# Performance work log

Hardware: AMD Instinct MI355X
Metric: run time of the kernel (lower is better)

Reference implementation:

```python
import jax, jax.numpy as jnp
import numpy as np

# Solver constants matching init_kwargs
DX = 2.0 / 128.0        # c_delta_x (domain [-1,1], 128 coarse cells)
DT = 1e-3               # c_delta_t
T_STAR = 0.064          # delta_t_star
NT = int(round(T_STAR / DT))  # 64 velocity-Verlet steps


def peri_laplacian(v, dx):
    """5-point Laplacian with periodic BC on last two axes."""
    return (jnp.roll(v, 1, -1) - 2.0 * v + jnp.roll(v, -1, -1)
            + jnp.roll(v, 1, -2) - 2.0 * v + jnp.roll(v, -1, -2)) / (dx * dx)


def grad2func(vx, vy, dx, sumv):
    """Recover u from its gradient components (wx, wy) via FFT inversion.
    vx, vy: [B, H, W]; sumv sets the DC (mean) mode."""
    ny, nx = vx.shape[-2], vx.shape[-1]
    kx = (2.0 * jnp.pi) * jnp.fft.fftfreq(nx, d=dx).astype(vx.dtype)  # [W]
    ky = (2.0 * jnp.pi) * jnp.fft.fftfreq(ny, d=dx).astype(vx.dtype)  # [H]
    KX = kx[None, :]
    KY = ky[:, None]
    rad = KX ** 2 + KY ** 2
    rad = rad.at[0, 0].set(1.0)
    hatx = jnp.fft.fft2(vx)
    haty = jnp.fft.fft2(vy)
    hatv = -1j * (hatx * KX + haty * KY) / rad
    hatv = hatv.at[..., 0, 0].set(sumv.astype(hatv.dtype))
    return jnp.real(jnp.fft.ifft2(hatv))


def wave_sol_from_energy(wx, wy, wtc, c, dx, sumv):
    u = grad2func(wx, wy, dx, sumv)
    ut = wtc * c
    return u, ut


def velocity_verlet(u, ut, c, dx, dt, nt):
    """nt steps of velocity Verlet for u_tt = c^2 * Lap(u), periodic BC."""
    c2 = c * c
    def step(carry, _):
        u, ut = carry
        lap0 = peri_laplacian(u, dx)
        u_new = u + dt * ut + 0.5 * dt * dt * c2 * lap0
        lap1 = peri_laplacian(u_new, dx)
        ut_new = ut + 0.5 * dt * c2 * (lap0 + lap1)
        return (u_new, ut_new), None
    (u, ut), _ = jax.lax.scan(step, (u, ut), None, length=nt)
    return u, ut


def wave_energy_components(u, ut, c, dx):
    wx = jnp.zeros_like(u).at[..., :, 1:].set((u[..., :, 1:] - u[..., :, :-1]) / dx)
    wy = jnp.zeros_like(u).at[..., 1:, :].set((u[..., 1:, :] - u[..., :-1, :]) / dx)
    wtc = ut / c
    return wx, wy, wtc


def setup_inputs() -> dict:
    key = jax.random.key(0)
    k1, k2 = jax.random.split(key)
    B, H, W = 16, 256, 256
    # channels 0..2: energy components (small-amplitude fields)
    fields = 0.1 * jax.random.normal(k1, (B, 3, H, W), dtype=jnp.float32)
    # channel 3: wave speed, strictly positive (divided by / squared in solver)
    vel = jax.random.uniform(k2, (B, 1, H, W), dtype=jnp.float32,
                             minval=1.0, maxval=3.0)
    restr_output = jnp.concatenate([fields, vel], axis=1)  # [B, 4, H, W]
    return {"restr_output": restr_output}


def reference(restr_output) -> jnp.ndarray:
    wx = restr_output[:, 0]
    wy = restr_output[:, 1]
    wtc = restr_output[:, 2]
    vel_c = restr_output[:, 3]
    # faithful to original: scalar sum of wx over the ENTIRE batch
    sumv = jnp.sum(wx)
    u, ut = wave_sol_from_energy(wx, wy, wtc, vel_c, DX, sumv)
    u, ut = velocity_verlet(u, ut, vel_c, DX, DT, NT)
    wx2, wy2, wtc2 = wave_energy_components(u, ut, vel_c, DX)
    return jnp.stack((wx2, wy2, wtc2, vel_c), axis=1)  # [B, 4, H, W]
```

## Files before the change

kernel.cpp:

```cpp
#include <hip/hip_runtime.h>

#define NBATCH 16
#define NPIX   65536
#define NTOT   (NBATCH * NPIX)

constexpr float DTf    = 0.001f;
constexpr float HDTf   = 0.0005f;
constexpr float HDT2f  = 5.0000000000000004e-07f;
constexpr float INV_DX  = 64.0f;
constexpr float INV_DX2 = 4096.0f;
constexpr float TWO_PI  = 6.28318530717958647692f;

constexpr int FWD = -1;
constexpr int INV =  1;

__device__ __forceinline__ void fft256_stockham(float* ar, float* ai,
                                                float* br, float* bi,
                                                const float* twr, const float* twi,
                                                int lane)
{
  float *xr = ar, *xi = ai, *yr = br, *yi = bi;
#pragma unroll
  for (int s = 0; s < 8; ++s) {
    const int m = 1 << s;
    __syncthreads();
#pragma unroll
    for (int q = 0; q < 2; ++q) {
      const int b  = lane + (q << 6);
      const int jm = b & ~(m - 1);
      const float wr = twr[jm], wi = twi[jm];
      const float c0r = xr[b],       c0i = xi[b];
      const float c1r = xr[b + 128], c1i = xi[b + 128];
      const int i0 = b + jm, i1 = i0 + m;
      yr[i0] = c0r + c1r;
      yi[i0] = c0i + c1i;
      const float dr = c0r - c1r, di = c0i - c1i;
      yr[i1] = wr * dr - wi * di;
      yi[i1] = wr * di + wi * dr;
    }
    float* t;
    t = xr; xr = yr; yr = t;
    t = xi; xi = yi; yi = t;
  }
  __syncthreads();
}

__global__ __launch_bounds__(512) void k_fwd_rows_pack(const float* __restrict__ in,
                                                       float2* __restrict__ A,
                                                       float* __restrict__ sum)
{
  __shared__ float ar[8 * 256], ai[8 * 256], br[8 * 256], bi[8 * 256];
  __shared__ float twr[128], twi[128];
  __shared__ float part[8];
  const int tid = threadIdx.x;
  const int lane = tid & 63;
  const int wv = tid >> 6;
  const int row0 = blockIdx.x << 3;

  float acc = 0.0f;
  for (int i = tid; i < 2048; i += 512) {
    const int r = i >> 8, e = i & 255;
    const int row = row0 + r;
    const int b = row >> 8, y = row & 255;
    const float vx = in[((size_t)(b << 2) << 16) + (y << 8) + e];
    const float vy = in[((size_t)((b << 2) | 1) << 16) + (y << 8) + e];
    ar[(r << 8) + e] = vx; acc += vx;
    ai[(r << 8) + e] = vy;
  }
  for (int t = tid; t < 128; t += 512) {
    float s, c;
    sincosf((float)FWD * (TWO_PI / 256.0f) * (float)t, &s, &c);
    twr[t] = c; twi[t] = s;
  }
#pragma unroll
  for (int o = 32; o > 0; o >>= 1) acc += __shfl_down(acc, o);
  if (lane == 0) part[wv] = acc;
  __syncthreads();
  if (tid == 0) {
    float s = part[0];
#pragma unroll
    for (int w = 1; w < 8; ++w) s += part[w];
    atomicAdd(sum, s);
  }

  fft256_stockham(ar + (wv << 8), ai + (wv << 8), br + (wv << 8), bi + (wv << 8),
                  twr, twi, lane);

  for (int i = tid; i < 2048; i += 512) {
    const int r = i >> 8, e = i & 255;
    A[((size_t)(row0 + r) << 8) + e] = make_float2(ar[(r << 8) + e], ai[(r << 8) + e]);
  }
}

__global__ __launch_bounds__(512) void k_fft_cols_panel_fwd(float2* __restrict__ X)
{
  constexpr int CS = 260;
  __shared__ float ar[8 * CS], ai[8 * CS], br[8 * CS], bi[8 * CS];
  __shared__ float twr[128], twi[128];
  const int tid = threadIdx.x;
  const int lane = tid & 63;
  const int wv = tid >> 6;
  const int b = blockIdx.x >> 5;
  const int x0 = (blockIdx.x & 31) << 3;
  float2* base = X + ((size_t)b << 16) + x0;

  for (int i = tid; i < 2048; i += 512) {
    const int row = i >> 3, c = i & 7;
    const float2 v = base[(row << 8) + c];
    ar[c * CS + row] = v.x;
    ai[c * CS + row] = v.y;
  }
  for (int t = tid; t < 128; t += 512) {
    float s, c;
    sincosf((float)FWD * (TWO_PI / 256.0f) * (float)t, &s, &c);
    twr[t] = c; twi[t] = s;
  }
  fft256_stockham(ar + wv * CS, ai + wv * CS, br + wv * CS, bi + wv * CS,
                  twr, twi, lane);
  for (int i = tid; i < 2048; i += 512) {
    const int row = i >> 3, c = i & 7;
    base[(row << 8) + c] = make_float2(ar[c * CS + row], ai[c * CS + row]);
  }
}

__global__ __launch_bounds__(512) void k_combine_invcol(const float2* __restrict__ A,
                                                        const float* __restrict__ sum,
                                                        float2* __restrict__ Bf)
{
  constexpr int CS = 260;
  __shared__ float ar[8 * CS], ai[8 * CS], br[8 * CS], bi[8 * CS];
  __shared__ float twr[128], twi[128];
  const int tid = threadIdx.x;
  const int lane = tid & 63;
  const int wv = tid >> 6;
  const int b = blockIdx.x >> 5;
  const int x0 = (blockIdx.x & 31) << 3;
  const float2* Ab = A + ((size_t)b << 16);

  for (int i = tid; i < 2048; i += 512) {
    const int ky = i >> 3, c = i & 7;
    const int kx = x0 + c;
    const float2 Zk = Ab[(ky << 8) + kx];
    const int ky2 = (256 - ky) & 255, kx2 = (256 - kx) & 255;
    const float2 Zm = Ab[(ky2 << 8) + kx2];
    const float Xr = 0.5f * (Zk.x + Zm.x), Xi = 0.5f * (Zk.y - Zm.y);
    const float Yr = 0.5f * (Zk.y + Zm.y), Yi = 0.5f * (Zm.x - Zk.x);
    const float fx = 0.25f * (float)(kx < 128 ? kx : kx - 256);
    const float fy = 0.25f * (float)(ky < 128 ? ky : ky - 256);
    const float kxv = TWO_PI * fx, kyv = TWO_PI * fy;
    float re, im;
    if ((ky | kx) == 0) {
      re = sum[0]; im = 0.0f;
    } else {
      const float rad = kxv * kxv + kyv * kyv;
      const float sr = Xr * kxv + Yr * kyv;
      const float si = Xi * kxv + Yi * kyv;
      re = si / rad; im = -sr / rad;
    }
    ar[c * CS + ky] = re;
    ai[c * CS + ky] = im;
  }
  for (int t = tid; t < 128; t += 512) {
    float s, c;
    sincosf((float)INV * (TWO_PI / 256.0f) * (float)t, &s, &c);
    twr[t] = c; twi[t] = s;
  }
  fft256_stockham(ar + wv * CS, ai + wv * CS, br + wv * CS, bi + wv * CS,
                  twr, twi, lane);
  float2* ob = Bf + ((size_t)b << 16) + x0;
  for (int i = tid; i < 2048; i += 512) {
    const int row = i >> 3, c = i & 7;
    ob[(row << 8) + c] = make_float2(ar[c * CS + row], ai[c * CS + row]);
  }
}

__global__ __launch_bounds__(512) void k_inv_rows_extract(const float2* __restrict__ Bf,
                                                          const float* __restrict__ in,
                                                          float* __restrict__ u,
                                                          float* __restrict__ ut)
{
  __shared__ float ar[8 * 256], ai[8 * 256], br[8 * 256], bi[8 * 256];
  __shared__ float twr[128], twi[128];
  const int tid = threadIdx.x;
  const int lane = tid & 63;
  const int wv = tid >> 6;
  const int row0 = blockIdx.x << 3;

  for (int i = tid; i < 2048; i += 512) {
    const int r = i >> 8, e = i & 255;
    const float2 v = Bf[((size_t)(row0 + r) << 8) + e];
    ar[(r << 8) + e] = v.x;
    ai[(r << 8) + e] = v.y;
  }
  for (int t = tid; t < 128; t += 512) {
    float s, c;
    sincosf((float)INV * (TWO_PI / 256.0f) * (float)t, &s, &c);
    twr[t] = c; twi[t] = s;
  }
  fft256_stockham(ar + (wv << 8), ai + (wv << 8), br + (wv << 8), bi + (wv << 8),
                  twr, twi, lane);

  for (int i = tid; i < 2048; i += 512) {
    const int r = i >> 8, e = i & 255;
    const int row = row0 + r;
    const int b = row >> 8, y = row & 255;
    const float wtc = in[((size_t)((b << 2) | 2) << 16) + (y << 8) + e];
    const float vc  = in[((size_t)((b << 2) | 3) << 16) + (y << 8) + e];
    u [((size_t)row << 8) + e] = ar[(r << 8) + e] * (1.0f / 65536.0f);
    ut[((size_t)row << 8) + e] = wtc * vc;
  }
}

template <int FINAL>
__global__ __launch_bounds__(256, 4) void k_verlet8(const float* __restrict__ u_in,
                                                    const float* __restrict__ ut_in,
                                                    const float* __restrict__ in,
                                                    float* __restrict__ u_out,
                                                    float* __restrict__ ut_out,
                                                    float* __restrict__ out)
{
  __shared__ float su[50 * 51];
  __shared__ float tmp[48 * 49];
  const int tid = threadIdx.x;
  const int b = blockIdx.x >> 6, t = blockIdx.x & 63;
  const int ty0 = (t >> 3) << 5, tx0 = (t & 7) << 5;
  const int ty = tid >> 4, tx = tid & 15;
  const int y0 = 1 + 3 * ty, x0 = 1 + 3 * tx;
  const float* ub  = u_in  + ((size_t)b << 16);
  const float* utb = ut_in + ((size_t)b << 16);
  const float* vb  = in + ((size_t)((b << 2) | 3) << 16);

  for (int i = tid; i < 2500; i += 256) {
    const int iy = i / 50, ix = i - iy * 50;
    const int gy = (ty0 + iy - 9) & 255, gx = (tx0 + ix - 9) & 255;
    su[iy * 51 + ix] = ub[(gy << 8) + gx];
  }
  for (int i = tid; i < 2304; i += 256) {
    const int iy = i / 48, ix = i - iy * 48;
    const int gy = (ty0 + iy - 8) & 255, gx = (tx0 + ix - 8) & 255;
    tmp[iy * 49 + ix] = utb[(gy << 8) + gx];
  }
  __syncthreads();

  float uR[3][3], utR[3][3], c2R[3][3], laR[3][3];
#pragma unroll
  for (int r = 0; r < 3; ++r)
#pragma unroll
    for (int c = 0; c < 3; ++c) {
      uR[r][c]  = su[(y0 + r) * 51 + x0 + c];
      utR[r][c] = tmp[(3 * ty + r) * 49 + 3 * tx + c];
    }
  __syncthreads();
  for (int i = tid; i < 2304; i += 256) {
    const int iy = i / 48, ix = i - iy * 48;
    const int gy = (ty0 + iy - 8) & 255, gx = (tx0 + ix - 8) & 255;
    tmp[iy * 49 + ix] = vb[(gy << 8) + gx];
  }
  __syncthreads();
#pragma unroll
  for (int r = 0; r < 3; ++r)
#pragma unroll
    for (int c = 0; c < 3; ++c) {
      const float cv = tmp[(3 * ty + r) * 49 + 3 * tx + c];
      c2R[r][c] = cv * cv;
    }

  float hN[3], hS[3], hW[3], hE[3];
  auto load_halo = [&]() {
#pragma unroll
    for (int c = 0; c < 3; ++c) {
      hN[c] = su[(y0 - 1) * 51 + x0 + c];
      hS[c] = su[(y0 + 3) * 51 + x0 + c];
    }
#pragma unroll
    for (int r = 0; r < 3; ++r) {
      hW[r] = su[(y0 + r) * 51 + x0 - 1];
      hE[r] = su[(y0 + r) * 51 + x0 + 3];
    }
  };
  auto lap_cell = [&](int r, int c) -> float {
    const float v = uR[r][c];
    const float L = (c == 0) ? hW[r] : uR[r][c - 1];
    const float R = (c == 2) ? hE[r] : uR[r][c + 1];
    const float U = (r == 0) ? hN[c] : uR[r - 1][c];
    const float D = (r == 2) ? hS[c] : uR[r + 1][c];
    const float t2 = 2.0f * v;
    return (((((L - t2) + R) + U) - t2) + D) * INV_DX2;
  };

  load_halo();
#pragma unroll
  for (int r = 0; r < 3; ++r)
#pragma unroll
    for (int c = 0; c < 3; ++c) laR[r][c] = lap_cell(r, c);
  __syncthreads();

  for (int j = 0; j < 8; ++j) {
#pragma unroll
    for (int r = 0; r < 3; ++r)
#pragma unroll
      for (int c = 0; c < 3; ++c)
        uR[r][c] = (uR[r][c] + DTf * utR[r][c]) + (HDT2f * c2R[r][c]) * laR[r][c];
    su[(y0    ) * 51 + x0    ] = uR[0][0];
    su[(y0    ) * 51 + x0 + 1] = uR[0][1];
    su[(y0    ) * 51 + x0 + 2] = uR[0][2];
    su[(y0 + 1) * 51 + x0    ] = uR[1][0];
    su[(y0 + 1) * 51 + x0 + 2] = uR[1][2];
    su[(y0 + 2) * 51 + x0    ] = uR[2][0];
    su[(y0 + 2) * 51 + x0 + 1] = uR[2][1];
    su[(y0 + 2) * 51 + x0 + 2] = uR[2][2];
    __syncthreads();
    load_halo();
#pragma unroll
    for (int r = 0; r < 3; ++r)
#pragma unroll
      for (int c = 0; c < 3; ++c) {
        const float ln = lap_cell(r, c);
        utR[r][c] = utR[r][c] + (HDTf * c2R[r][c]) * (laR[r][c] + ln);
        laR[r][c] = ln;
      }
    __syncthreads();
  }

#pragma unroll
  for (int r = 0; r < 3; ++r)
#pragma unroll
    for (int c = 0; c < 3; ++c) su[(y0 + r) * 51 + x0 + c] = uR[r][c];
  __syncthreads();

  if (FINAL) {
    float wxv[4], wyv[4];
#pragma unroll
    for (int k = 0; k < 4; ++k) {
      const int i = tid + (k << 8);
      const int oy = i >> 5, ox = i & 31;
      const float uc = su[(9 + oy) * 51 + 9 + ox];
      wxv[k] = (tx0 + ox == 0) ? 0.0f : (uc - su[(9 + oy) * 51 + 8 + ox]) * INV_DX;
      wyv[k] = (ty0 + oy == 0) ? 0.0f : (uc - su[(8 + oy) * 51 + 9 + ox]) * INV_DX;
    }
    __syncthreads();
#pragma unroll
    for (int r = 0; r < 3; ++r)
#pragma unroll
      for (int c = 0; c < 3; ++c) su[(y0 + r) * 51 + x0 + c] = utR[r][c];
    __syncthreads();
#pragma unroll
    for (int k = 0; k < 4; ++k) {
      const int i = tid + (k << 8);
      const int oy = i >> 5, ox = i & 31;
      const int g = ((ty0 + oy) << 8) + (tx0 + ox);
      const float utv = su[(9 + oy) * 51 + 9 + ox];
      const float cv  = vb[g];
      out[((size_t)(b << 2) << 16) + g]       = wxv[k];
      out[((size_t)((b << 2) | 1) << 16) + g] = wyv[k];
      out[((size_t)((b << 2) | 2) << 16) + g] = utv / cv;
      out[((size_t)((b << 2) | 3) << 16) + g] = cv;
    }
  } else {
    float* uob  = u_out  + ((size_t)b << 16);
    float* utob = ut_out + ((size_t)b << 16);
    for (int i = tid; i < 1024; i += 256) {
      const int oy = i >> 5, ox = i & 31;
      uob[((ty0 + oy) << 8) + tx0 + ox] = su[(9 + oy) * 51 + 9 + ox];
    }
    __syncthreads();
#pragma unroll
    for (int r = 0; r < 3; ++r)
#pragma unroll
      for (int c = 0; c < 3; ++c) su[(y0 + r) * 51 + x0 + c] = utR[r][c];
    __syncthreads();
    for (int i = tid; i < 1024; i += 256) {
      const int oy = i >> 5, ox = i & 31;
      utob[((ty0 + oy) << 8) + tx0 + ox] = su[(9 + oy) * 51 + 9 + ox];
    }
  }
}

extern "C" void kernel_launch(void* const* d_in, const int* in_sizes, int n_in,
                              void* d_out, int out_size, void* d_ws, size_t ws_size,
                              hipStream_t stream)
{
  const float* in = (const float*)d_in[0];
  float* out = (float*)d_out;
  char* ws = (char*)d_ws;

  float2* A   = (float2*)d_out;
  float*  u1  = (float*)d_out;
  float*  ut1 = u1 + NTOT;
  float2* Bf  = (float2*)((float*)d_out + 2 * NTOT);

  float*  sum = (float*)ws;
  float*  u0  = (float*)ws;
  float*  ut0 = u0 + NTOT;

  hipMemsetAsync(sum, 0, sizeof(float), stream);

  k_fwd_rows_pack<<<NBATCH * 32, 512, 0, stream>>>(in, A, sum);
  k_fft_cols_panel_fwd<<<NBATCH * 32, 512, 0, stream>>>(A);
  k_combine_invcol<<<NBATCH * 32, 512, 0, stream>>>(A, sum, Bf);
  k_inv_rows_extract<<<NBATCH * 32, 512, 0, stream>>>(Bf, in, u1, ut1);

  for (int s = 0; s < 7; ++s) {
    if (s & 1) k_verlet8<0><<<NBATCH * 64, 256, 0, stream>>>(u0, ut0, in, u1, ut1, out);
    else       k_verlet8<0><<<NBATCH * 64, 256, 0, stream>>>(u1, ut1, in, u0, ut0, out);
  }
  k_verlet8<1><<<NBATCH * 64, 256, 0, stream>>>(u0, ut0, in, u1, ut1, out);
}
```

Measured before the change: 259.6 us.

## Fuse column FFT with spectral combine; double-buffer Verlet shared tile

```diff
diff --git a/kernel.cpp b/kernel.cpp
--- a/kernel.cpp
+++ b/kernel.cpp
@@ -92,44 +92,13 @@
   }
 }
 
-__global__ __launch_bounds__(512) void k_fft_cols_panel_fwd(float2* __restrict__ X)
+__global__ __launch_bounds__(1024) void k_cols_fused(const float2* __restrict__ A,
+                                                     const float* __restrict__ sum,
+                                                     float2* __restrict__ Bf)
 {
   constexpr int CS = 260;
-  __shared__ float ar[8 * CS], ai[8 * CS], br[8 * CS], bi[8 * CS];
-  __shared__ float twr[128], twi[128];
-  const int tid = threadIdx.x;
-  const int lane = tid & 63;
-  const int wv = tid >> 6;
-  const int b = blockIdx.x >> 5;
-  const int x0 = (blockIdx.x & 31) << 3;
-  float2* base = X + ((size_t)b << 16) + x0;
-
-  for (int i = tid; i < 2048; i += 512) {
-    const int row = i >> 3, c = i & 7;
-    const float2 v = base[(row << 8) + c];
-    ar[c * CS + row] = v.x;
-    ai[c * CS + row] = v.y;
-  }
-  for (int t = tid; t < 128; t += 512) {
-    float s, c;
-    sincosf((float)FWD * (TWO_PI / 256.0f) * (float)t, &s, &c);
-    twr[t] = c; twi[t] = s;
-  }
-  fft256_stockham(ar + wv * CS, ai + wv * CS, br + wv * CS, bi + wv * CS,
-                  twr, twi, lane);
-  for (int i = tid; i < 2048; i += 512) {
-    const int row = i >> 3, c = i & 7;
-    base[(row << 8) + c] = make_float2(ar[c * CS + row], ai[c * CS + row]);
-  }
-}
-
-__global__ __launch_bounds__(512) void k_combine_invcol(const float2* __restrict__ A,
-                                                        const float* __restrict__ sum,
-                                                        float2* __restrict__ Bf)
-{
-  constexpr int CS = 260;
-  __shared__ float ar[8 * CS], ai[8 * CS], br[8 * CS], bi[8 * CS];
-  __shared__ float twr[128], twi[128];
+  __shared__ float ar[16 * CS], ai[16 * CS], br[16 * CS], bi[16 * CS];
+  __shared__ float twfr[128], twfi[128], twvr[128], twvi[128];
   const int tid = threadIdx.x;
   const int lane = tid & 63;
   const int wv = tid >> 6;
@@ -137,14 +106,31 @@
   const int x0 = (blockIdx.x & 31) << 3;
   const float2* Ab = A + ((size_t)b << 16);
 
-  for (int i = tid; i < 2048; i += 512) {
+  for (int i = tid; i < 4096; i += 1024) {
+    const int row = i >> 4, c = i & 15;
+    const int col = (c < 8) ? (x0 + c) : ((256 - (x0 + (c - 8))) & 255);
+    const float2 v = Ab[(row << 8) + col];
+    ar[c * CS + row] = v.x;
+    ai[c * CS + row] = v.y;
+  }
+  for (int t = tid; t < 128; t += 1024) {
+    float s, c;
+    sincosf((float)FWD * (TWO_PI / 256.0f) * (float)t, &s, &c);
+    twfr[t] = c; twfi[t] = s;
+    twvr[t] = c; twvi[t] = -s;
+  }
+
+  fft256_stockham(ar + wv * CS, ai + wv * CS, br + wv * CS, bi + wv * CS,
+                  twfr, twfi, lane);
+
+  for (int i = tid; i < 2048; i += 1024) {
     const int ky = i >> 3, c = i & 7;
     const int kx = x0 + c;
-    const float2 Zk = Ab[(ky << 8) + kx];
-    const int ky2 = (256 - ky) & 255, kx2 = (256 - kx) & 255;
-    const float2 Zm = Ab[(ky2 << 8) + kx2];
-    const float Xr = 0.5f * (Zk.x + Zm.x), Xi = 0.5f * (Zk.y - Zm.y);
-    const float Yr = 0.5f * (Zk.y + Zm.y), Yi = 0.5f * (Zm.x - Zk.x);
+    const int ky2 = (256 - ky) & 255;
+    const float Zkr = ar[c * CS + ky],        Zki = ai[c * CS + ky];
+    const float Zmr = ar[(8 + c) * CS + ky2], Zmi = ai[(8 + c) * CS + ky2];
+    const float Xr = 0.5f * (Zkr + Zmr), Xi = 0.5f * (Zki - Zmi);
+    const float Yr = 0.5f * (Zki + Zmi), Yi = 0.5f * (Zmr - Zkr);
     const float fx = 0.25f * (float)(kx < 128 ? kx : kx - 256);
     const float fy = 0.25f * (float)(ky < 128 ? ky : ky - 256);
     const float kxv = TWO_PI * fx, kyv = TWO_PI * fy;
@@ -157,20 +143,18 @@
       const float si = Xi * kxv + Yi * kyv;
       re = si / rad; im = -sr / rad;
     }
-    ar[c * CS + ky] = re;
-    ai[c * CS + ky] = im;
-  }
-  for (int t = tid; t < 128; t += 512) {
-    float s, c;
-    sincosf((float)INV * (TWO_PI / 256.0f) * (float)t, &s, &c);
-    twr[t] = c; twi[t] = s;
-  }
-  fft256_stockham(ar + wv * CS, ai + wv * CS, br + wv * CS, bi + wv * CS,
-                  twr, twi, lane);
+    br[c * CS + ky] = re;
+    bi[c * CS + ky] = im;
+  }
+
+  const int s8 = wv & 7;
+  fft256_stockham(br + s8 * CS, bi + s8 * CS, ar + s8 * CS, ai + s8 * CS,
+                  twvr, twvi, lane);
+
   float2* ob = Bf + ((size_t)b << 16) + x0;
-  for (int i = tid; i < 2048; i += 512) {
+  for (int i = tid; i < 2048; i += 1024) {
     const int row = i >> 3, c = i & 7;
-    ob[(row << 8) + c] = make_float2(ar[c * CS + row], ai[c * CS + row]);
+    ob[(row << 8) + c] = make_float2(br[c * CS + row], bi[c * CS + row]);
   }
 }
 
@@ -219,7 +203,8 @@
                                                     float* __restrict__ ut_out,
                                                     float* __restrict__ out)
 {
-  __shared__ float su[50 * 51];
+  __shared__ float suA[50 * 51];
+  __shared__ float suB[50 * 51];
   __shared__ float tmp[48 * 49];
   const int tid = threadIdx.x;
   const int b = blockIdx.x >> 6, t = blockIdx.x & 63;
@@ -233,7 +218,7 @@
   for (int i = tid; i < 2500; i += 256) {
     const int iy = i / 50, ix = i - iy * 50;
     const int gy = (ty0 + iy - 9) & 255, gx = (tx0 + ix - 9) & 255;
-    su[iy * 51 + ix] = ub[(gy << 8) + gx];
+    suA[iy * 51 + ix] = ub[(gy << 8) + gx];
   }
   for (int i = tid; i < 2304; i += 256) {
     const int iy = i / 48, ix = i - iy * 48;
@@ -247,7 +232,7 @@
   for (int r = 0; r < 3; ++r)
 #pragma unroll
     for (int c = 0; c < 3; ++c) {
-      uR[r][c]  = su[(y0 + r) * 51 + x0 + c];
+      uR[r][c]  = suA[(y0 + r) * 51 + x0 + c];
       utR[r][c] = tmp[(3 * ty + r) * 49 + 3 * tx + c];
     }
   __syncthreads();
@@ -266,16 +251,16 @@
     }
 
   float hN[3], hS[3], hW[3], hE[3];
-  auto load_halo = [&]() {
+  auto load_halo = [&](const float* U) {
 #pragma unroll
     for (int c = 0; c < 3; ++c) {
-      hN[c] = su[(y0 - 1) * 51 + x0 + c];
-      hS[c] = su[(y0 + 3) * 51 + x0 + c];
+      hN[c] = U[(y0 - 1) * 51 + x0 + c];
+      hS[c] = U[(y0 + 3) * 51 + x0 + c];
     }
 #pragma unroll
     for (int r = 0; r < 3; ++r) {
-      hW[r] = su[(y0 + r) * 51 + x0 - 1];
-      hE[r] = su[(y0 + r) * 51 + x0 + 3];
+      hW[r] = U[(y0 + r) * 51 + x0 - 1];
+      hE[r] = U[(y0 + r) * 51 + x0 + 3];
     }
   };
   auto lap_cell = [&](int r, int c) -> float {
@@ -288,29 +273,29 @@
     return (((((L - t2) + R) + U) - t2) + D) * INV_DX2;
   };
 
-  load_halo();
+  load_halo(suA);
 #pragma unroll
   for (int r = 0; r < 3; ++r)
 #pragma unroll
     for (int c = 0; c < 3; ++c) laR[r][c] = lap_cell(r, c);
-  __syncthreads();
 
   for (int j = 0; j < 8; ++j) {
+    float* W = (j & 1) ? suA : suB;
 #pragma unroll
     for (int r = 0; r < 3; ++r)
 #pragma unroll
       for (int c = 0; c < 3; ++c)
         uR[r][c] = (uR[r][c] + DTf * utR[r][c]) + (HDT2f * c2R[r][c]) * laR[r][c];
-    su[(y0    ) * 51 + x0    ] = uR[0][0];
-    su[(y0    ) * 51 + x0 + 1] = uR[0][1];
-    su[(y0    ) * 51 + x0 + 2] = uR[0][2];
-    su[(y0 + 1) * 51 + x0    ] = uR[1][0];
-    su[(y0 + 1) * 51 + x0 + 2] = uR[1][2];
-    su[(y0 + 2) * 51 + x0    ] = uR[2][0];
-    su[(y0 + 2) * 51 + x0 + 1] = uR[2][1];
-    su[(y0 + 2) * 51 + x0 + 2] = uR[2][2];
-    __syncthreads();
-    load_halo();
+    W[(y0    ) * 51 + x0    ] = uR[0][0];
+    W[(y0    ) * 51 + x0 + 1] = uR[0][1];
+    W[(y0    ) * 51 + x0 + 2] = uR[0][2];
+    W[(y0 + 1) * 51 + x0    ] = uR[1][0];
+    W[(y0 + 1) * 51 + x0 + 2] = uR[1][2];
+    W[(y0 + 2) * 51 + x0    ] = uR[2][0];
+    W[(y0 + 2) * 51 + x0 + 1] = uR[2][1];
+    W[(y0 + 2) * 51 + x0 + 2] = uR[2][2];
+    __syncthreads();
+    load_halo(W);
 #pragma unroll
     for (int r = 0; r < 3; ++r)
 #pragma unroll
@@ -319,13 +304,12 @@
         utR[r][c] = utR[r][c] + (HDTf * c2R[r][c]) * (laR[r][c] + ln);
         laR[r][c] = ln;
       }
-    __syncthreads();
   }
 
 #pragma unroll
   for (int r = 0; r < 3; ++r)
 #pragma unroll
-    for (int c = 0; c < 3; ++c) su[(y0 + r) * 51 + x0 + c] = uR[r][c];
+    for (int c = 0; c < 3; ++c) suB[(y0 + r) * 51 + x0 + c] = uR[r][c];
   __syncthreads();
 
   if (FINAL) {
@@ -334,22 +318,22 @@
     for (int k = 0; k < 4; ++k) {
       const int i = tid + (k << 8);
       const int oy = i >> 5, ox = i & 31;
-      const float uc = su[(9 + oy) * 51 + 9 + ox];
-      wxv[k] = (tx0 + ox == 0) ? 0.0f : (uc - su[(9 + oy) * 51 + 8 + ox]) * INV_DX;
-      wyv[k] = (ty0 + oy == 0) ? 0.0f : (uc - su[(8 + oy) * 51 + 9 + ox]) * INV_DX;
+      const float uc = suB[(9 + oy) * 51 + 9 + ox];
+      wxv[k] = (tx0 + ox == 0) ? 0.0f : (uc - suB[(9 + oy) * 51 + 8 + ox]) * INV_DX;
+      wyv[k] = (ty0 + oy == 0) ? 0.0f : (uc - suB[(8 + oy) * 51 + 9 + ox]) * INV_DX;
     }
     __syncthreads();
 #pragma unroll
     for (int r = 0; r < 3; ++r)
 #pragma unroll
-      for (int c = 0; c < 3; ++c) su[(y0 + r) * 51 + x0 + c] = utR[r][c];
+      for (int c = 0; c < 3; ++c) suB[(y0 + r) * 51 + x0 + c] = utR[r][c];
     __syncthreads();
 #pragma unroll
     for (int k = 0; k < 4; ++k) {
       const int i = tid + (k << 8);
       const int oy = i >> 5, ox = i & 31;
       const int g = ((ty0 + oy) << 8) + (tx0 + ox);
-      const float utv = su[(9 + oy) * 51 + 9 + ox];
+      const float utv = suB[(9 + oy) * 51 + 9 + ox];
       const float cv  = vb[g];
       out[((size_t)(b << 2) << 16) + g]       = wxv[k];
       out[((size_t)((b << 2) | 1) << 16) + g] = wyv[k];
@@ -361,17 +345,17 @@
     float* utob = ut_out + ((size_t)b << 16);
     for (int i = tid; i < 1024; i += 256) {
       const int oy = i >> 5, ox = i & 31;
-      uob[((ty0 + oy) << 8) + tx0 + ox] = su[(9 + oy) * 51 + 9 + ox];
+      uob[((ty0 + oy) << 8) + tx0 + ox] = suB[(9 + oy) * 51 + 9 + ox];
     }
     __syncthreads();
 #pragma unroll
     for (int r = 0; r < 3; ++r)
 #pragma unroll
-      for (int c = 0; c < 3; ++c) su[(y0 + r) * 51 + x0 + c] = utR[r][c];
+      for (int c = 0; c < 3; ++c) suB[(y0 + r) * 51 + x0 + c] = utR[r][c];
     __syncthreads();
     for (int i = tid; i < 1024; i += 256) {
       const int oy = i >> 5, ox = i & 31;
-      utob[((ty0 + oy) << 8) + tx0 + ox] = su[(9 + oy) * 51 + 9 + ox];
+      utob[((ty0 + oy) << 8) + tx0 + ox] = suB[(9 + oy) * 51 + 9 + ox];
     }
   }
 }
@@ -396,8 +380,7 @@
   hipMemsetAsync(sum, 0, sizeof(float), stream);
 
   k_fwd_rows_pack<<<NBATCH * 32, 512, 0, stream>>>(in, A, sum);
-  k_fft_cols_panel_fwd<<<NBATCH * 32, 512, 0, stream>>>(A);
-  k_combine_invcol<<<NBATCH * 32, 512, 0, stream>>>(A, sum, Bf);
+  k_cols_fused<<<NBATCH * 32, 1024, 0, stream>>>(A, sum, Bf);
   k_inv_rows_extract<<<NBATCH * 32, 512, 0, stream>>>(Bf, in, u1, ut1);
 
   for (int s = 0; s < 7; ++s) {
```

New measurement: 255.7 us. No clear change (-1.5%).
